# Optimization experiments

Hardware: AMD Instinct MI355X
Metric: run time of the kernel (lower is better)

The kernel has to match this reference:

```python
import jax, jax.numpy as jnp
import numpy as np

B, S, E, H, DH, F, L, C = 32, 197, 768, 12, 64, 2048, 4, 1000
LN_EPS = 1e-5


def setup_inputs() -> dict:
    key = jax.random.key(0)
    ks = jax.random.split(key, 16)
    sc = 0.02
    return {
        "x": jax.random.normal(ks[0], (B, S, E), dtype=jnp.float32),
        "Wk": jax.random.normal(ks[1], (L, H, E, DH), dtype=jnp.float32) * sc,
        "Wq": jax.random.normal(ks[2], (L, H, E, DH), dtype=jnp.float32) * sc,
        "Wv": jax.random.normal(ks[3], (L, H, E, DH), dtype=jnp.float32) * sc,
        "Wconv": jax.random.normal(ks[4], (L, H * DH, E), dtype=jnp.float32) * sc,
        "ln1_w": jnp.ones((L, E), jnp.float32),
        "ln1_b": jnp.zeros((L, E), jnp.float32),
        "ln2_w": jnp.ones((L, E), jnp.float32),
        "ln2_b": jnp.zeros((L, E), jnp.float32),
        "W1": jax.random.normal(ks[5], (L, E, F), dtype=jnp.float32) * sc,
        "b1": jnp.zeros((L, F), jnp.float32),
        "W2": jax.random.normal(ks[6], (L, F, E), dtype=jnp.float32) * sc,
        "b2": jnp.zeros((L, E), jnp.float32),
        "Wc": jax.random.normal(ks[7], (E, C), dtype=jnp.float32) * sc,
        "bc": jnp.zeros((C,), jnp.float32),
    }


def _layernorm(x, w, b):
    mu = jnp.mean(x, axis=-1, keepdims=True)
    var = jnp.mean(jnp.square(x - mu), axis=-1, keepdims=True)
    return (x - mu) * jax.lax.rsqrt(var + LN_EPS) * w + b


def reference(x, Wk, Wq, Wv, Wconv, ln1_w, ln1_b, ln2_w, ln2_b, W1, b1, W2, b2, Wc, bc):
    # NOTE: original scales attention scores by sqrt(seq_len), not sqrt(d_k)
    seq_len = x.shape[1]
    inv_scale = 1.0 / jnp.sqrt(jnp.float32(seq_len))
    h = x
    for l in range(L):  # small fixed layer loop
        xn = _layernorm(h, ln1_w[l], ln1_b[l])
        q = jnp.einsum('bse,hed->bhsd', xn, Wq[l])
        k = jnp.einsum('bse,hed->bhsd', xn, Wk[l])
        v = jnp.einsum('bse,hed->bhsd', xn, Wv[l])
        scores = jnp.einsum('bhsd,bhtd->bhst', q, k) * inv_scale
        att = jax.nn.softmax(scores, axis=-1)
        o = jnp.einsum('bhst,bhtd->bhsd', att, v)
        # concat heads: b s (h d), head index outermost in last dim
        o = o.transpose(0, 2, 1, 3).reshape(o.shape[0], o.shape[2], H * DH)
        mha = o @ Wconv[l]
        res1 = mha + h
        xn2 = _layernorm(res1, ln2_w[l], ln2_b[l])
        ff = jax.nn.gelu(xn2 @ W1[l] + b1[l], approximate=False) @ W2[l] + b2[l]
        h = ff + res1
    logits = h[:, 0] @ Wc + bc
    return jax.nn.softmax(logits, axis=-1)
```

## Files before the change

### kernel.cpp

```cpp
#include <hip/hip_runtime.h>
#include <hip/hip_bf16.h>
#include <math.h>

#define BQ 32
#define SQ 197
#define EQ 768
#define HQ 12
#define DHQ 64
#define FQ 2048
#define LQ 4
#define CQ 1000
#define BSQ (BQ*SQ)
#define SP 208
#define S16 13
#define MP (BQ*SP)
#define QKV3 2304
#define KTP 7
#define LN_EPS 1e-5f

typedef __bf16 bf16x8 __attribute__((ext_vector_type(8)));
typedef float f32x4 __attribute__((ext_vector_type(4)));
typedef unsigned short u16x8 __attribute__((ext_vector_type(8)));

typedef const __attribute__((address_space(1))) unsigned int* gas_t;
typedef __attribute__((address_space(3))) unsigned int* las_t;

__device__ __forceinline__ __hip_bfloat16 tobf(float f) { return __float2bfloat16(f); }

__device__ __forceinline__ size_t pk(int rt, int KT, int kt, int lane) {
    return (((size_t)rt * KT + kt) * 64 + (size_t)lane) * 8;
}

#define QPK_SLAB (S16*2*512)
#define QPK_TOT  ((size_t)BQ*HQ*QPK_SLAB + 4096)
#define VPK_SLAB (4*KTP*512)
#define VPK_TOT  ((size_t)BQ*HQ*VPK_SLAB + 4096)
#define LWSLAB (4*(size_t)EQ*EQ + 2*(size_t)EQ*FQ)

template<int N>
__device__ __forceinline__ void waitvm() {
    asm volatile("s_waitcnt vmcnt(%0)" :: "n"(N) : "memory");
}
__device__ __forceinline__ void barx() {
    asm volatile("" ::: "memory");
    __builtin_amdgcn_s_barrier();
    asm volatile("" ::: "memory");
}
__device__ __forceinline__ void lds_fence() {
    asm volatile("s_waitcnt lgkmcnt(0)" ::: "memory");
    __builtin_amdgcn_sched_barrier(0);
}

__device__ __forceinline__ float gelu_f(float v) {
    float ax = fabsf(v) * 0.70710678118654752f;
    float t  = __builtin_amdgcn_rcpf(1.0f + 0.3275911f * ax);
    float p  = ((((1.061405429f * t - 1.453152027f) * t + 1.421413741f) * t
               - 0.284496736f) * t + 0.254829592f) * t;
    float e  = __expf(-ax * ax);
    float er = 1.0f - p * e;
    return v * (0.5f * (1.0f + copysignf(er, v)));
}

__global__ __launch_bounds__(256) void copy_pad(const float* __restrict__ x,
    float* __restrict__ bh)
{
    int r = blockIdx.x;
    int b = r / SP, s = r - b * SP;
    float* dst = bh + (size_t)r * EQ;
    int t = threadIdx.x;
    if (s < SQ) {
        const float* src = x + ((size_t)b * SQ + s) * EQ;
        dst[t]       = src[t];
        dst[t + 256] = src[t + 256];
        dst[t + 512] = src[t + 512];
    } else {
        dst[t] = 0.f; dst[t + 256] = 0.f; dst[t + 512] = 0.f;
    }
}

__device__ __forceinline__ void tconv_body(const float* __restrict__ ip,
    unsigned short* __restrict__ out, int C, int KT, int ntb_base, int r0, int c0)
{
    __shared__ float tile[64][65];
    int t = threadIdx.x;
    int tc = t & 63, tr = t >> 6;
    #pragma unroll
    for (int p = 0; p < 16; ++p) {
        int r = p * 4 + tr;
        tile[r][tc] = ip[(size_t)(r0 + r) * C + c0 + tc];
    }
    __syncthreads();
    int ntb = ntb_base + (c0 >> 4);
    int ktb = r0 >> 5;
    #pragma unroll
    for (int p = 0; p < 2; ++p) {
        int cc = p * 256 + t;
        int lane = cc & 63, grp = cc >> 6;
        int ktl = grp & 1, ntl = grp >> 1;
        int er = ktl * 32 + (lane >> 4) * 8;
        int dc = ntl * 16 + (lane & 15);
        u16x8 v;
        #pragma unroll
        for (int e = 0; e < 8; ++e) {
            __hip_bfloat16 h = tobf(tile[er + e][dc]);
            v[e] = *(unsigned short*)&h;
        }
        *(u16x8*)(out + pk(ntb + ntl, KT, ktb + ktl, lane)) = v;
    }
}

__global__ __launch_bounds__(256) void tconv_all(
    const float* __restrict__ Wq, const float* __restrict__ Wk,
    const float* __restrict__ Wv, const float* __restrict__ Wcv,
    const float* __restrict__ W1, const float* __restrict__ W2,
    unsigned short* __restrict__ wAll)
{
    int id = blockIdx.x;
    const int l = id / 1344; id -= l * 1344;
    unsigned short* wl = wAll + (size_t)l * LWSLAB;
    const float* src; unsigned short* dst;
    int C, KT, ntb, r0, c0;
    if (id < 432) {
        int x = id % 12, z = id / 12;
        int which = z / 12, zz = z - which * 12;
        const float* s0 = (which == 0) ? Wq : (which == 1) ? Wk : Wv;
        src = s0 + ((size_t)l * HQ + zz) * EQ * DHQ;
        dst = wl + (size_t)which * EQ * EQ;
        C = DHQ; KT = 24; ntb = zz * 4; r0 = x * 64; c0 = 0;
    } else if (id < 576) {
        int t = id - 432;
        src = Wcv + (size_t)l * EQ * EQ;
        dst = wl + 3 * (size_t)EQ * EQ;
        C = EQ; KT = 24; ntb = 0; r0 = (t % 12) * 64; c0 = (t / 12) * 64;
    } else if (id < 960) {
        int t = id - 576;
        src = W1 + (size_t)l * EQ * FQ;
        dst = wl + 4 * (size_t)EQ * EQ;
        C = FQ; KT = 24; ntb = 0; r0 = (t % 12) * 64; c0 = (t / 12) * 64;
    } else {
        int t = id - 960;
        src = W2 + (size_t)l * FQ * EQ;
        dst = wl + 4 * (size_t)EQ * EQ + (size_t)EQ * FQ;
        C = EQ; KT = 64; ntb = 0; r0 = (t % 32) * 64; c0 = (t / 32) * 64;
    }
    tconv_body(src, dst, C, KT, ntb, r0, c0);
}

__global__ __launch_bounds__(256) void ln_kernel(const float* __restrict__ in,
    const float* __restrict__ w, const float* __restrict__ b,
    unsigned short* __restrict__ out)
{
    const int wv = threadIdx.x >> 6, L = threadIdx.x & 63;
    const int row = blockIdx.x * 4 + wv;
    const float* x = in + (size_t)row * EQ;
    float4 a0 = *(const float4*)(x + 8 * L);
    float4 a1 = *(const float4*)(x + 8 * L + 4);
    float4 a2 = make_float4(0.f, 0.f, 0.f, 0.f), a3 = a2;
    const bool two = (L < 32);
    if (two) {
        a2 = *(const float4*)(x + 512 + 8 * L);
        a3 = *(const float4*)(x + 512 + 8 * L + 4);
    }
    float s = a0.x + a0.y + a0.z + a0.w + a1.x + a1.y + a1.z + a1.w
            + a2.x + a2.y + a2.z + a2.w + a3.x + a3.y + a3.z + a3.w;
    #pragma unroll
    for (int d = 1; d < 64; d <<= 1) s += __shfl_xor(s, d);
    const float mu = s * (1.0f / EQ);
    float q = (a0.x-mu)*(a0.x-mu) + (a0.y-mu)*(a0.y-mu) + (a0.z-mu)*(a0.z-mu) + (a0.w-mu)*(a0.w-mu)
            + (a1.x-mu)*(a1.x-mu) + (a1.y-mu)*(a1.y-mu) + (a1.z-mu)*(a1.z-mu) + (a1.w-mu)*(a1.w-mu);
    if (two)
        q += (a2.x-mu)*(a2.x-mu) + (a2.y-mu)*(a2.y-mu) + (a2.z-mu)*(a2.z-mu) + (a2.w-mu)*(a2.w-mu)
           + (a3.x-mu)*(a3.x-mu) + (a3.y-mu)*(a3.y-mu) + (a3.z-mu)*(a3.z-mu) + (a3.w-mu)*(a3.w-mu);
    #pragma unroll
    for (int d = 1; d < 64; d <<= 1) q += __shfl_xor(q, d);
    const float rs = rsqrtf(q * (1.0f / EQ) + LN_EPS);

    const int rt = row >> 4, rsl = row & 15;
    auto store_chunk = [&](int c, float4 v0, float4 v1) {
        int kt = c >> 2, c2 = c & 3;
        int lane2 = (c2 << 4) + rsl;
        int k0 = c << 3;
        float4 w0 = *(const float4*)(w + k0), w1 = *(const float4*)(w + k0 + 4);
        float4 g0 = *(const float4*)(b + k0), g1 = *(const float4*)(b + k0 + 4);
        float va[8] = {v0.x, v0.y, v0.z, v0.w, v1.x, v1.y, v1.z, v1.w};
        float wa[8] = {w0.x, w0.y, w0.z, w0.w, w1.x, w1.y, w1.z, w1.w};
        float ba[8] = {g0.x, g0.y, g0.z, g0.w, g1.x, g1.y, g1.z, g1.w};
        u16x8 o;
        #pragma unroll
        for (int e = 0; e < 8; ++e) {
            __hip_bfloat16 h = tobf((va[e] - mu) * rs * wa[e] + ba[e]);
            o[e] = *(unsigned short*)&h;
        }
        *(u16x8*)(out + pk(rt, 24, kt, lane2)) = o;
    };
    store_chunk(L, a0, a1);
    if (two) store_chunk(64 + L, a2, a3);
}

template<int KT, int RT>
__device__ __forceinline__ void kloop_staged(
    const unsigned short* __restrict__ Apk,
    const unsigned short* __restrict__ Bpk,
    int rtb, int ntb, int tid, unsigned short* sm, f32x4 (&acc)[RT][4])
{
    static_assert(KT >= 3, "need >=3 k-tiles");
    constexpr int AC  = RT * 2;
    constexpr int NCH = AC + 8;
    constexpr int CPW = NCH / 4;
    const int lane = tid & 63, w = tid >> 6;
    const int wr = w >> 1, wc = w & 1;
    const int cbase = w * CPW;

    const unsigned short* sp[CPW];
    #pragma unroll
    for (int q = 0; q < CPW; ++q) {
        int c = cbase + q;
        sp[q] = (c < AC) ? Apk + pk(rtb + c, KT, 0, lane)
                         : Bpk + pk(ntb + (c - AC), KT, 0, lane);
    }
    unsigned short* bufs0 = sm;
    unsigned short* bufs1 = sm + NCH * 512;
    unsigned short* bufs2 = sm + 2 * NCH * 512;

    auto stagef = [&](unsigned short* dst) {
        #pragma unroll
        for (int q = 0; q < CPW; ++q) {
            __builtin_amdgcn_global_load_lds(
                (gas_t)sp[q], (las_t)(dst + (cbase + q) * 512), 16, 0, 0);
            sp[q] += 512;
        }
    };
    auto frags = [&](const unsigned short* cur, bf16x8 (&af)[RT], bf16x8 (&bb)[4]) {
        #pragma unroll
        for (int i = 0; i < RT; ++i)
            af[i] = *(const bf16x8*)(cur + (wr * RT + i) * 512 + lane * 8);
        #pragma unroll
        for (int j = 0; j < 4; ++j)
            bb[j] = *(const bf16x8*)(cur + (AC + wc * 4 + j) * 512 + lane * 8);
    };
    auto mf = [&](bf16x8 (&af)[RT], bf16x8 (&bb)[4]) {
        #pragma unroll
        for (int i = 0; i < RT; ++i)
            #pragma unroll
            for (int j = 0; j < 4; ++j)
                acc[i][j] = __builtin_amdgcn_mfma_f32_16x16x32_bf16(af[i], bb[j], acc[i][j], 0, 0, 0);
    };

    stagef(bufs0);
    stagef(bufs1);
    unsigned short *cur = bufs0, *nxt = bufs1, *nx2 = bufs2;

    #pragma unroll 1
    for (int kt = 0; kt < KT - 2; ++kt) {
        waitvm<CPW>();
        barx();
        bf16x8 af[RT], bb[4];
        frags(cur, af, bb);
        stagef(nx2);
        mf(af, bb);
        unsigned short* t_ = cur; cur = nxt; nxt = nx2; nx2 = t_;
    }
    {
        waitvm<CPW>();
        barx();
        bf16x8 af[RT], bb[4];
        frags(cur, af, bb);
        mf(af, bb);
        cur = nxt;
    }
    {
        waitvm<0>();
        barx();
        bf16x8 af[RT], bb[4];
        frags(cur, af, bb);
        mf(af, bb);
    }
}

enum { EPI_NONE = 0, EPI_RES = 1, EPI_BIAS_GELU = 2, EPI_BIAS_RES = 3, EPI_QKV = 4 };

template<int EPI, int KT, int RT>
__global__ __launch_bounds__(256, 3) void mgemm_pk(
    const unsigned short* __restrict__ Apk, const unsigned short* __restrict__ Bpk,
    void* __restrict__ Cm, const float* __restrict__ bias,
    const float* __restrict__ res, int N, int nNT)
{
    constexpr int NCH = RT * 2 + 8;
    __shared__ __align__(16) unsigned short smem[(3 * NCH * 1024) / 2];

    const int nRowT = (RT == 4) ? 52 : 104;
    const int g = blockIdx.x & 7;
    const int sIdx = blockIdx.x >> 3;
    const int b0 = (nRowT * g) >> 3, b1 = (nRowT * (g + 1)) >> 3;
    const int colT = sIdx % nNT, rloc = sIdx / nNT;
    if (b0 + rloc >= b1) return;
    const int row0 = (b0 + rloc) * (RT * 32), col0 = colT << 7;

    const int tid = threadIdx.x;
    const int lane = tid & 63;
    const int w = tid >> 6;
    const int wr = w >> 1, wc = w & 1;
    const int l15 = lane & 15, quad = lane >> 4;

    f32x4 acc[RT][4] = {};
    kloop_staged<KT, RT>(Apk, Bpk, row0 >> 4, col0 >> 4, tid, smem, acc);

    if constexpr (EPI == EPI_BIAS_GELU) {
        __syncthreads();
        auto Cs = (unsigned short (*)[136])smem;
        #pragma unroll
        for (int j = 0; j < 4; ++j) {
            float bv = bias[col0 + wc * 64 + j * 16 + l15];
            #pragma unroll
            for (int i = 0; i < RT; ++i)
                #pragma unroll
                for (int rg = 0; rg < 4; ++rg) {
                    float v = gelu_f(acc[i][j][rg] + bv);
                    __hip_bfloat16 h = tobf(v);
                    Cs[wr * 64 + i * 16 + quad * 4 + rg][wc * 64 + j * 16 + l15] =
                        *(unsigned short*)&h;
                }
        }
        __syncthreads();
        const int KT2 = N >> 5;
        #pragma unroll
        for (int p = 0; p < 8; ++p) {
            int cc = p * 256 + tid;
            int ln2 = cc & 63, grp = cc >> 6;
            int ktl = grp & 3, rtl = grp >> 2;
            int rowl = rtl * 16 + (ln2 & 15);
            u16x8 v;
            #pragma unroll
            for (int e = 0; e < 8; ++e)
                v[e] = Cs[rowl][ktl * 32 + (ln2 >> 4) * 8 + e];
            *(u16x8*)((unsigned short*)Cm + pk((row0 >> 4) + rtl, KT2, (col0 >> 5) + ktl, ln2)) = v;
        }
    } else if constexpr (EPI == EPI_QKV) {
        unsigned short* qpk = (unsigned short*)Cm;
        unsigned short* kpk = (unsigned short*)(void*)bias;
        unsigned short* vpk = (unsigned short*)(void*)res;
        __syncthreads();
        auto Cs = (unsigned short (*)[136])smem;
        #pragma unroll
        for (int j = 0; j < 4; ++j)
            #pragma unroll
            for (int i = 0; i < 4; ++i)
                #pragma unroll
                for (int rg = 0; rg < 4; ++rg) {
                    __hip_bfloat16 h = tobf(acc[i][j][rg]);
                    Cs[wr * 64 + i * 16 + quad * 4 + rg][wc * 64 + j * 16 + l15] =
                        *(unsigned short*)&h;
                }
        __syncthreads();

        const int treg = col0 >> 7;
        if (treg < 12) {
            unsigned short* dst = (treg < 6) ? qpk : kpk;
            const int h0 = ((col0 % 768) >> 6);
            #pragma unroll
            for (int p = 0; p < 8; ++p) {
                int cc = p * 256 + tid;
                int ln2 = cc & 63, grp = cc >> 6;
                int hl = grp & 1, kt = (grp >> 1) & 1, rtl = grp >> 2;
                int row16 = (row0 >> 4) + rtl;
                int bb = row16 / S16;
                int s16 = row16 - bb * S16;
                int h = h0 + hl;
                u16x8 v;
                #pragma unroll
                for (int e = 0; e < 8; ++e)
                    v[e] = Cs[rtl * 16 + (ln2 & 15)][hl * 64 + kt * 32 + (ln2 >> 4) * 8 + e];
                *(u16x8*)(dst + ((((size_t)(bb * HQ + h) * S16 + s16) * 2 + kt) << 9) + ln2 * 8) = v;
            }
        } else {
            const int h0 = (col0 - 1536) >> 6;
            #pragma unroll
            for (int p = 0; p < 8; ++p) {
                int cc = p * 256 + tid;
                int dloc = cc & 127;
                int g8 = cc >> 7;
                int gr = row0 + g8 * 8;
                int bb = gr / SP;
                int tl = gr - bb * SP;
                int tt = tl >> 5;
                int tsub = (tl >> 3) & 3;
                int h = h0 + (dloc >> 6);
                int dt = (dloc >> 4) & 3;
                int lane2 = tsub * 16 + (dloc & 15);
                u16x8 v;
                #pragma unroll
                for (int e = 0; e < 8; ++e)
                    v[e] = Cs[g8 * 8 + e][dloc];
                *(u16x8*)(vpk + (size_t)(bb * HQ + h) * VPK_SLAB + pk(dt, KTP, tt, lane2)) = v;
            }
        }
    } else {
        #pragma unroll
        for (int j = 0; j < 4; ++j) {
            int c = col0 + wc * 64 + j * 16 + l15;
            float bv = (EPI == EPI_BIAS_RES) ? bias[c] : 0.f;
            #pragma unroll
            for (int i = 0; i < RT; ++i)
                #pragma unroll
                for (int rg = 0; rg < 4; ++rg) {
                    int r = row0 + wr * (RT * 16) + i * 16 + quad * 4 + rg;
                    float v = acc[i][j][rg];
                    size_t idx = (size_t)r * N + c;
                    if (EPI == EPI_BIAS_RES) {
                        ((float*)Cm)[idx] = v + bv + res[idx];
                    } else if (EPI == EPI_RES) {
                        ((float*)Cm)[idx] = v + res[idx];
                    } else {
                        ((__hip_bfloat16*)Cm)[idx] = tobf(v);
                    }
                }
        }
    }
}

__global__ __launch_bounds__(128, 4) void attn_fused(
    const unsigned short* __restrict__ qpk, const unsigned short* __restrict__ kpk,
    const unsigned short* __restrict__ vpk, unsigned short* __restrict__ opk)
{
    __shared__ unsigned short Ps[2][16][240];
    __shared__ unsigned short Cs[2][16][72];
    const int bh = blockIdx.x;
    const int b = bh / HQ, h = bh - b * HQ;
    const int tid = threadIdx.x;
    const int w = tid >> 6, lane = tid & 63;
    const int l15 = lane & 15, quad = lane >> 4;
    const int rt = blockIdx.y * 2 + w;
    if (rt >= S16) return;

    const unsigned short* qs = qpk + (size_t)bh * QPK_SLAB;
    const unsigned short* ks = kpk + (size_t)bh * QPK_SLAB;
    const unsigned short* vs = vpk + (size_t)bh * VPK_SLAB;

    bf16x8 af0 = *(const bf16x8*)(qs + ((rt * 2 + 0) << 9) + lane * 8);
    bf16x8 af1 = *(const bf16x8*)(qs + ((rt * 2 + 1) << 9) + lane * 8);

    f32x4 acc[13] = {};
    bf16x8 kc0 = *(const bf16x8*)(ks + (0 << 9) + lane * 8);
    bf16x8 kc1 = *(const bf16x8*)(ks + (1 << 9) + lane * 8);
    #pragma unroll
    for (int j = 0; j < 13; ++j) {
        bf16x8 kn0, kn1;
        if (j + 1 < 13) {
            kn0 = *(const bf16x8*)(ks + (((j + 1) * 2 + 0) << 9) + lane * 8);
            kn1 = *(const bf16x8*)(ks + (((j + 1) * 2 + 1) << 9) + lane * 8);
        }
        __builtin_amdgcn_s_setprio(1);
        acc[j] = __builtin_amdgcn_mfma_f32_16x16x32_bf16(af0, kc0, acc[j], 0, 0, 0);
        acc[j] = __builtin_amdgcn_mfma_f32_16x16x32_bf16(af1, kc1, acc[j], 0, 0, 0);
        __builtin_amdgcn_s_setprio(0);
        kc0 = kn0; kc1 = kn1;
    }

    bf16x8 vb[4];
    #pragma unroll
    for (int d = 0; d < 4; ++d)
        vb[d] = *(const bf16x8*)(vs + pk(d, KTP, 0, lane));

    const float scale = 0.07124704998790965f;
    const int xr = (quad & 2) << 3;
    const unsigned short zbf = 0;
    float inv[4];
    #pragma unroll
    for (int rg = 0; rg < 4; ++rg) {
        float y[13];
        float m = -1e30f;
        #pragma unroll
        for (int j = 0; j < 13; ++j) {
            float v = acc[j][rg] * scale;
            if (j == 12) v = (l15 < 5) ? v : -1e30f;
            y[j] = v;
            m = fmaxf(m, v);
        }
        #pragma unroll
        for (int d = 1; d < 16; d <<= 1) m = fmaxf(m, __shfl_xor(m, d));
        float s = 0.f;
        #pragma unroll
        for (int j = 0; j < 13; ++j) {
            float e = __expf(y[j] - m);
            s += e;
            __hip_bfloat16 hv = tobf(e);
            Ps[w][quad * 4 + rg][(j * 16 + l15) ^ xr] = *(unsigned short*)&hv;
        }
        Ps[w][quad * 4 + rg][(208 + l15) ^ xr] = zbf;
        #pragma unroll
        for (int d = 1; d < 16; d <<= 1) s += __shfl_xor(s, d);
        inv[rg] = 1.0f / s;
    }
    lds_fence();

    f32x4 av[4] = {};
    #pragma unroll
    for (int kk = 0; kk < KTP; ++kk) {
        bf16x8 vn[4];
        if (kk + 1 < KTP) {
            #pragma unroll
            for (int d = 0; d < 4; ++d)
                vn[d] = *(const bf16x8*)(vs + pk(d, KTP, kk + 1, lane));
        }
        int col = (kk * 32 + quad * 8) ^ ((l15 & 8) << 1);
        bf16x8 pf = *(const bf16x8*)&Ps[w][l15][col];
        __builtin_amdgcn_s_setprio(1);
        #pragma unroll
        for (int d = 0; d < 4; ++d)
            av[d] = __builtin_amdgcn_mfma_f32_16x16x32_bf16(pf, vb[d], av[d], 0, 0, 0);
        __builtin_amdgcn_s_setprio(0);
        #pragma unroll
        for (int d = 0; d < 4; ++d) vb[d] = vn[d];
    }

    #pragma unroll
    for (int d = 0; d < 4; ++d)
        #pragma unroll
        for (int rg = 0; rg < 4; ++rg) {
            __hip_bfloat16 hv = tobf(av[d][rg] * inv[rg]);
            Cs[w][quad * 4 + rg][d * 16 + l15] = *(unsigned short*)&hv;
        }
    lds_fence();

    const int rtg = b * S16 + rt;
    #pragma unroll
    for (int ktl = 0; ktl < 2; ++ktl) {
        u16x8 v;
        #pragma unroll
        for (int e = 0; e < 8; ++e)
            v[e] = Cs[w][l15][ktl * 32 + quad * 8 + e];
        *(u16x8*)(opk + pk(rtg, 24, h * 2 + ktl, lane)) = v;
    }
}

__global__ __launch_bounds__(256) void logits_kernel(
    const float* __restrict__ hbuf, const float* __restrict__ Wc,
    const float* __restrict__ bc, float* __restrict__ logits)
{
    __shared__ __align__(16) float hs[768];
    __shared__ float red[256];
    int b = blockIdx.y;
    int tid = threadIdx.x;
    const float* hr = hbuf + (size_t)b * SP * EQ;
    for (int p = tid; p < 192; p += 256)
        *(float4*)&hs[p << 2] = *(const float4*)(hr + (p << 2));
    __syncthreads();
    int cl = tid & 31, ks = tid >> 5;
    int c = blockIdx.x * 32 + cl;
    int cs = (c < CQ) ? c : 0;
    float s = 0.f;
    int e0 = ks * 96;
    #pragma unroll 8
    for (int e = 0; e < 96; ++e)
        s = fmaf(hs[e0 + e], Wc[(size_t)(e0 + e) * CQ + cs], s);
    red[tid] = s;
    __syncthreads();
    for (int off = 128; off >= 32; off >>= 1) {
        if (tid < off) red[tid] += red[tid + off];
        __syncthreads();
    }
    if (tid < 32 && c < CQ)
        logits[(size_t)b * CQ + c] = red[tid] + bc[c];
}

__global__ __launch_bounds__(256) void smax_kernel(
    const float* __restrict__ logits, float* __restrict__ out)
{
    __shared__ float red[256];
    int b = blockIdx.x;
    int t = threadIdx.x;
    const float* lp = logits + (size_t)b * CQ;
    float lg[4];
    #pragma unroll
    for (int j = 0; j < 4; ++j) {
        int c = t + j * 256;
        lg[j] = (c < CQ) ? lp[c] : -1e30f;
    }
    float m = fmaxf(fmaxf(lg[0], lg[1]), fmaxf(lg[2], lg[3]));
    red[t] = m;
    __syncthreads();
    for (int off = 128; off; off >>= 1) {
        if (t < off) red[t] = fmaxf(red[t], red[t + off]);
        __syncthreads();
    }
    m = red[0];
    __syncthreads();
    float ex[4], s = 0.f;
    #pragma unroll
    for (int j = 0; j < 4; ++j) {
        ex[j] = (t + j * 256 < CQ) ? __expf(lg[j] - m) : 0.f;
        s += ex[j];
    }
    red[t] = s;
    __syncthreads();
    for (int off = 128; off; off >>= 1) {
        if (t < off) red[t] += red[t + off];
        __syncthreads();
    }
    float inv = 1.0f / red[0];
    #pragma unroll
    for (int j = 0; j < 4; ++j)
        if (t + j * 256 < CQ) out[(size_t)b * CQ + t + j * 256] = ex[j] * inv;
}

extern "C" void kernel_launch(void* const* d_in, const int* in_sizes, int n_in,
                              void* d_out, int out_size, void* d_ws, size_t ws_size,
                              hipStream_t stream)
{
    const float* x     = (const float*)d_in[0];
    const float* Wk    = (const float*)d_in[1];
    const float* Wq    = (const float*)d_in[2];
    const float* Wv    = (const float*)d_in[3];
    const float* Wconv = (const float*)d_in[4];
    const float* ln1w  = (const float*)d_in[5];
    const float* ln1b  = (const float*)d_in[6];
    const float* ln2w  = (const float*)d_in[7];
    const float* ln2b  = (const float*)d_in[8];
    const float* W1    = (const float*)d_in[9];
    const float* b1    = (const float*)d_in[10];
    const float* W2    = (const float*)d_in[11];
    const float* b2    = (const float*)d_in[12];
    const float* Wc    = (const float*)d_in[13];
    const float* bc    = (const float*)d_in[14];
    float* out = (float*)d_out;

    const size_t MPE = (size_t)MP * EQ;

    float* w = (float*)d_ws;
    float* bh    = w; w += MPE;
    float* res1  = w; w += MPE;
    float* logit = w; w += (size_t)BQ * CQ;
    unsigned short* qpk  = (unsigned short*)w;
    unsigned short* kpk  = qpk + QPK_TOT;
    unsigned short* vpk  = kpk + QPK_TOT;
    unsigned short* actb = vpk + VPK_TOT;
    unsigned short* ffh  = actb + MPE;
    unsigned short* wAll = ffh + (size_t)MP * FQ;

    copy_pad<<<MP, 256, 0, stream>>>(x, bh);
    tconv_all<<<4 * 1344, 256, 0, stream>>>(Wq, Wk, Wv, Wconv, W1, W2, wAll);

    for (int l = 0; l < LQ; ++l) {
        unsigned short* wl   = wAll + (size_t)l * LWSLAB;
        unsigned short* WcvT = wl + 3 * (size_t)EQ * EQ;
        unsigned short* W1T  = wl + 4 * (size_t)EQ * EQ;
        unsigned short* W2T  = W1T + (size_t)EQ * FQ;

        ln_kernel<<<MP / 4, 256, 0, stream>>>(bh, ln1w + l * EQ, ln1b + l * EQ, actb);

        mgemm_pk<EPI_QKV, 24, 4><<<8 * 7 * 18, 256, 0, stream>>>(
            actb, wl, qpk, (const float*)kpk, (const float*)vpk, QKV3, 18);

        attn_fused<<<dim3(BQ * HQ, 7), 128, 0, stream>>>(qpk, kpk, vpk, actb);

        mgemm_pk<EPI_RES, 24, 4><<<8 * 7 * 6, 256, 0, stream>>>(
            actb, WcvT, res1, nullptr, bh, EQ, 6);

        ln_kernel<<<MP / 4, 256, 0, stream>>>(res1, ln2w + l * EQ, ln2b + l * EQ, actb);

        mgemm_pk<EPI_BIAS_GELU, 24, 4><<<8 * 7 * 16, 256, 0, stream>>>(
            actb, W1T, ffh, b1 + l * FQ, nullptr, FQ, 16);
        mgemm_pk<EPI_BIAS_RES, 64, 4><<<8 * 7 * 6, 256, 0, stream>>>(
            ffh, W2T, bh, b2 + l * EQ, res1, EQ, 6);
    }
    logits_kernel<<<dim3(32, BQ), 256, 0, stream>>>(bh, Wc, bc, logit);
    smax_kernel<<<BQ, 256, 0, stream>>>(logit, out);
}
```

Before: 734.6 us.

## Process two query row-tiles per attention wave and add dedicated FF2 GEMM

The attention kernel now gives each wave two 16-row query tiles. Every K and V fragment loaded is reused for two MFMA chains, which halves K/V global traffic per query row and cuts the grid from 7 to 4 y-blocks. This costs more registers and LDS, so the occupancy hint drops from 4 to 3. Separately, the second FFN GEMM moves to a specialized kernel with a fixed 128x128 tile, double-buffered global-to-LDS staging and a fused bias+residual epilogue, replacing the generic templated GEMM.

Result: slower. 771.0 us (+5.0%).

```diff
diff --git a/kernel.cpp b/kernel.cpp
--- a/kernel.cpp
+++ b/kernel.cpp
@@ -418,28 +418,116 @@
     }
 }
 
-__global__ __launch_bounds__(128, 4) void attn_fused(
+__global__ __launch_bounds__(256, 2) void mgemm_ff2(
+    const unsigned short* __restrict__ Apk, const unsigned short* __restrict__ Bpk,
+    float* __restrict__ Cm, const float* __restrict__ bias,
+    const float* __restrict__ res, int N, int nNT)
+{
+    __shared__ __align__(16) unsigned short smem[2 * 32 * 512];
+
+    const int g = blockIdx.x & 7;
+    const int sIdx = blockIdx.x >> 3;
+    const int b0 = (52 * g) >> 3, b1 = (52 * (g + 1)) >> 3;
+    const int colT = sIdx % nNT, rloc = sIdx / nNT;
+    if (b0 + rloc >= b1) return;
+    const int row0 = (b0 + rloc) * 128, col0 = colT << 7;
+
+    const int tid = threadIdx.x;
+    const int lane = tid & 63;
+    const int w = tid >> 6;
+    const int wr = w >> 1, wc = w & 1;
+    const int l15 = lane & 15, quad = lane >> 4;
+    const int rtb = row0 >> 4, ntb = col0 >> 4;
+
+    const unsigned short* sp[8];
+    #pragma unroll
+    for (int q = 0; q < 8; ++q) {
+        int c = w * 8 + q;
+        sp[q] = (c < 16) ? Apk + pk(rtb + (c >> 1), 64, c & 1, lane)
+                         : Bpk + pk(ntb + ((c - 16) >> 1), 64, c & 1, lane);
+    }
+    auto stagef = [&](unsigned short* dst) {
+        #pragma unroll
+        for (int q = 0; q < 8; ++q) {
+            __builtin_amdgcn_global_load_lds(
+                (gas_t)sp[q], (las_t)(dst + (w * 8 + q) * 512), 16, 0, 0);
+            sp[q] += 1024;
+        }
+    };
+
+    f32x4 acc[4][4] = {};
+    stagef(smem);
+    #pragma unroll 1
+    for (int s = 0; s < 32; ++s) {
+        waitvm<0>();
+        asm volatile("s_waitcnt lgkmcnt(0)" ::: "memory");
+        barx();
+        unsigned short* cur = smem + (s & 1) * 32 * 512;
+        bf16x8 af[4][2], bb[4][2];
+        #pragma unroll
+        for (int i = 0; i < 4; ++i)
+            #pragma unroll
+            for (int ktl = 0; ktl < 2; ++ktl)
+                af[i][ktl] = *(const bf16x8*)(cur + (((wr * 4 + i) << 1) + ktl) * 512 + lane * 8);
+        #pragma unroll
+        for (int j = 0; j < 4; ++j)
+            #pragma unroll
+            for (int ktl = 0; ktl < 2; ++ktl)
+                bb[j][ktl] = *(const bf16x8*)(cur + (16 + ((wc * 4 + j) << 1) + ktl) * 512 + lane * 8);
+        if (s + 1 < 32) stagef(smem + ((s + 1) & 1) * 32 * 512);
+        __builtin_amdgcn_s_setprio(1);
+        #pragma unroll
+        for (int ktl = 0; ktl < 2; ++ktl)
+            #pragma unroll
+            for (int i = 0; i < 4; ++i)
+                #pragma unroll
+                for (int j = 0; j < 4; ++j)
+                    acc[i][j] = __builtin_amdgcn_mfma_f32_16x16x32_bf16(af[i][ktl], bb[j][ktl], acc[i][j], 0, 0, 0);
+        __builtin_amdgcn_s_setprio(0);
+    }
+
+    #pragma unroll
+    for (int j = 0; j < 4; ++j) {
+        int c = col0 + wc * 64 + j * 16 + l15;
+        float bv = bias[c];
+        #pragma unroll
+        for (int i = 0; i < 4; ++i)
+            #pragma unroll
+            for (int rg = 0; rg < 4; ++rg) {
+                int r = row0 + wr * 64 + i * 16 + quad * 4 + rg;
+                size_t idx = (size_t)r * N + c;
+                Cm[idx] = acc[i][j][rg] + bv + res[idx];
+            }
+    }
+}
+
+__global__ __launch_bounds__(128, 3) void attn_fused(
     const unsigned short* __restrict__ qpk, const unsigned short* __restrict__ kpk,
     const unsigned short* __restrict__ vpk, unsigned short* __restrict__ opk)
 {
-    __shared__ unsigned short Ps[2][16][240];
-    __shared__ unsigned short Cs[2][16][72];
+    __shared__ unsigned short Ps[2][2][16][240];
+    __shared__ unsigned short Cs[2][2][16][72];
     const int bh = blockIdx.x;
     const int b = bh / HQ, h = bh - b * HQ;
     const int tid = threadIdx.x;
     const int w = tid >> 6, lane = tid & 63;
     const int l15 = lane & 15, quad = lane >> 4;
-    const int rt = blockIdx.y * 2 + w;
-    if (rt >= S16) return;
+    const int pr = blockIdx.y * 2 + w;
+    const int rta = pr * 2;
+    if (rta >= S16) return;
+    const int rtb = rta + 1;
+    const bool haveB = (rtb < S16);
 
     const unsigned short* qs = qpk + (size_t)bh * QPK_SLAB;
     const unsigned short* ks = kpk + (size_t)bh * QPK_SLAB;
     const unsigned short* vs = vpk + (size_t)bh * VPK_SLAB;
 
-    bf16x8 af0 = *(const bf16x8*)(qs + ((rt * 2 + 0) << 9) + lane * 8);
-    bf16x8 af1 = *(const bf16x8*)(qs + ((rt * 2 + 1) << 9) + lane * 8);
-
-    f32x4 acc[13] = {};
+    bf16x8 aa0 = *(const bf16x8*)(qs + ((rta * 2 + 0) << 9) + lane * 8);
+    bf16x8 aa1 = *(const bf16x8*)(qs + ((rta * 2 + 1) << 9) + lane * 8);
+    bf16x8 ab0 = *(const bf16x8*)(qs + ((rtb * 2 + 0) << 9) + lane * 8);
+    bf16x8 ab1 = *(const bf16x8*)(qs + ((rtb * 2 + 1) << 9) + lane * 8);
+
+    f32x4 acca[13] = {}, accb[13] = {};
     bf16x8 kc0 = *(const bf16x8*)(ks + (0 << 9) + lane * 8);
     bf16x8 kc1 = *(const bf16x8*)(ks + (1 << 9) + lane * 8);
     #pragma unroll
@@ -450,8 +538,10 @@
             kn1 = *(const bf16x8*)(ks + (((j + 1) * 2 + 1) << 9) + lane * 8);
         }
         __builtin_amdgcn_s_setprio(1);
-        acc[j] = __builtin_amdgcn_mfma_f32_16x16x32_bf16(af0, kc0, acc[j], 0, 0, 0);
-        acc[j] = __builtin_amdgcn_mfma_f32_16x16x32_bf16(af1, kc1, acc[j], 0, 0, 0);
+        acca[j] = __builtin_amdgcn_mfma_f32_16x16x32_bf16(aa0, kc0, acca[j], 0, 0, 0);
+        acca[j] = __builtin_amdgcn_mfma_f32_16x16x32_bf16(aa1, kc1, acca[j], 0, 0, 0);
+        accb[j] = __builtin_amdgcn_mfma_f32_16x16x32_bf16(ab0, kc0, accb[j], 0, 0, 0);
+        accb[j] = __builtin_amdgcn_mfma_f32_16x16x32_bf16(ab1, kc1, accb[j], 0, 0, 0);
         __builtin_amdgcn_s_setprio(0);
         kc0 = kn0; kc1 = kn1;
     }
@@ -464,36 +554,41 @@
     const float scale = 0.07124704998790965f;
     const int xr = (quad & 2) << 3;
     const unsigned short zbf = 0;
-    float inv[4];
-    #pragma unroll
-    for (int rg = 0; rg < 4; ++rg) {
-        float y[13];
-        float m = -1e30f;
-        #pragma unroll
-        for (int j = 0; j < 13; ++j) {
-            float v = acc[j][rg] * scale;
-            if (j == 12) v = (l15 < 5) ? v : -1e30f;
-            y[j] = v;
-            m = fmaxf(m, v);
-        }
-        #pragma unroll
-        for (int d = 1; d < 16; d <<= 1) m = fmaxf(m, __shfl_xor(m, d));
-        float s = 0.f;
-        #pragma unroll
-        for (int j = 0; j < 13; ++j) {
-            float e = __expf(y[j] - m);
-            s += e;
-            __hip_bfloat16 hv = tobf(e);
-            Ps[w][quad * 4 + rg][(j * 16 + l15) ^ xr] = *(unsigned short*)&hv;
-        }
-        Ps[w][quad * 4 + rg][(208 + l15) ^ xr] = zbf;
-        #pragma unroll
-        for (int d = 1; d < 16; d <<= 1) s += __shfl_xor(s, d);
-        inv[rg] = 1.0f / s;
+    float inva[4], invb[4];
+    #pragma unroll
+    for (int half = 0; half < 2; ++half) {
+        const f32x4* acc = half ? accb : acca;
+        float* inv = half ? invb : inva;
+        #pragma unroll
+        for (int rg = 0; rg < 4; ++rg) {
+            float y[13];
+            float m = -1e30f;
+            #pragma unroll
+            for (int j = 0; j < 13; ++j) {
+                float v = acc[j][rg] * scale;
+                if (j == 12) v = (l15 < 5) ? v : -1e30f;
+                y[j] = v;
+                m = fmaxf(m, v);
+            }
+            #pragma unroll
+            for (int d = 1; d < 16; d <<= 1) m = fmaxf(m, __shfl_xor(m, d));
+            float s = 0.f;
+            #pragma unroll
+            for (int j = 0; j < 13; ++j) {
+                float e = __expf(y[j] - m);
+                s += e;
+                __hip_bfloat16 hv = tobf(e);
+                Ps[w][half][quad * 4 + rg][(j * 16 + l15) ^ xr] = *(unsigned short*)&hv;
+            }
+            Ps[w][half][quad * 4 + rg][(208 + l15) ^ xr] = zbf;
+            #pragma unroll
+            for (int d = 1; d < 16; d <<= 1) s += __shfl_xor(s, d);
+            inv[rg] = 1.0f / s;
+        }
     }
     lds_fence();
 
-    f32x4 av[4] = {};
+    f32x4 ava[4] = {}, avb[4] = {};
     #pragma unroll
     for (int kk = 0; kk < KTP; ++kk) {
         bf16x8 vn[4];
@@ -503,11 +598,14 @@
                 vn[d] = *(const bf16x8*)(vs + pk(d, KTP, kk + 1, lane));
         }
         int col = (kk * 32 + quad * 8) ^ ((l15 & 8) << 1);
-        bf16x8 pf = *(const bf16x8*)&Ps[w][l15][col];
+        bf16x8 pa = *(const bf16x8*)&Ps[w][0][l15][col];
+        bf16x8 pb = *(const bf16x8*)&Ps[w][1][l15][col];
         __builtin_amdgcn_s_setprio(1);
         #pragma unroll
-        for (int d = 0; d < 4; ++d)
-            av[d] = __builtin_amdgcn_mfma_f32_16x16x32_bf16(pf, vb[d], av[d], 0, 0, 0);
+        for (int d = 0; d < 4; ++d) {
+            ava[d] = __builtin_amdgcn_mfma_f32_16x16x32_bf16(pa, vb[d], ava[d], 0, 0, 0);
+            avb[d] = __builtin_amdgcn_mfma_f32_16x16x32_bf16(pb, vb[d], avb[d], 0, 0, 0);
+        }
         __builtin_amdgcn_s_setprio(0);
         #pragma unroll
         for (int d = 0; d < 4; ++d) vb[d] = vn[d];
@@ -517,19 +615,25 @@
     for (int d = 0; d < 4; ++d)
         #pragma unroll
         for (int rg = 0; rg < 4; ++rg) {
-            __hip_bfloat16 hv = tobf(av[d][rg] * inv[rg]);
-            Cs[w][quad * 4 + rg][d * 16 + l15] = *(unsigned short*)&hv;
+            __hip_bfloat16 ha = tobf(ava[d][rg] * inva[rg]);
+            Cs[w][0][quad * 4 + rg][d * 16 + l15] = *(unsigned short*)&ha;
+            __hip_bfloat16 hb = tobf(avb[d][rg] * invb[rg]);
+            Cs[w][1][quad * 4 + rg][d * 16 + l15] = *(unsigned short*)&hb;
         }
     lds_fence();
 
-    const int rtg = b * S16 + rt;
-    #pragma unroll
-    for (int ktl = 0; ktl < 2; ++ktl) {
-        u16x8 v;
-        #pragma unroll
-        for (int e = 0; e < 8; ++e)
-            v[e] = Cs[w][l15][ktl * 32 + quad * 8 + e];
-        *(u16x8*)(opk + pk(rtg, 24, h * 2 + ktl, lane)) = v;
+    #pragma unroll
+    for (int half = 0; half < 2; ++half) {
+        if (half == 1 && !haveB) break;
+        const int rtg = b * S16 + rta + half;
+        #pragma unroll
+        for (int ktl = 0; ktl < 2; ++ktl) {
+            u16x8 v;
+            #pragma unroll
+            for (int e = 0; e < 8; ++e)
+                v[e] = Cs[w][half][l15][ktl * 32 + quad * 8 + e];
+            *(u16x8*)(opk + pk(rtg, 24, h * 2 + ktl, lane)) = v;
+        }
     }
 }
 
@@ -651,7 +755,7 @@
         mgemm_pk<EPI_QKV, 24, 4><<<8 * 7 * 18, 256, 0, stream>>>(
             actb, wl, qpk, (const float*)kpk, (const float*)vpk, QKV3, 18);
 
-        attn_fused<<<dim3(BQ * HQ, 7), 128, 0, stream>>>(qpk, kpk, vpk, actb);
+        attn_fused<<<dim3(BQ * HQ, 4), 128, 0, stream>>>(qpk, kpk, vpk, actb);
 
         mgemm_pk<EPI_RES, 24, 4><<<8 * 7 * 6, 256, 0, stream>>>(
             actb, WcvT, res1, nullptr, bh, EQ, 6);
@@ -660,7 +764,7 @@
 
         mgemm_pk<EPI_BIAS_GELU, 24, 4><<<8 * 7 * 16, 256, 0, stream>>>(
             actb, W1T, ffh, b1 + l * FQ, nullptr, FQ, 16);
-        mgemm_pk<EPI_BIAS_RES, 64, 4><<<8 * 7 * 6, 256, 0, stream>>>(
+        mgemm_ff2<<<8 * 7 * 6, 256, 0, stream>>>(
             ffh, W2T, bh, b2 + l * EQ, res1, EQ, 6);
     }
     logits_kernel<<<dim3(32, BQ), 256, 0, stream>>>(bh, Wc, bc, logit);
```
